# Optimization experiments

Hardware: AMD Instinct MI355X
Metric: run time of the kernel (lower is better)

## Reference

```python
import jax, jax.numpy as jnp
import numpy as np

N = 8192          # bbox_num
C = 2048          # in_channels
IC = C // 2       # inter_channels


def setup_inputs() -> dict:
    key = jax.random.key(0)
    ks = jax.random.split(key, 12)
    s_lin = 1.0 / np.sqrt(C)    # torch Linear init scale for fan_in=C
    s_w = 1.0 / np.sqrt(IC)     # for fan_in=IC
    return {
        "x": jax.random.normal(ks[0], (N, C), dtype=jnp.float32),
        "theta_w": jax.random.uniform(ks[1], (IC, C), jnp.float32, -s_lin, s_lin),
        "theta_b": jax.random.uniform(ks[2], (IC,), jnp.float32, -s_lin, s_lin),
        "phi_w": jax.random.uniform(ks[3], (IC, C), jnp.float32, -s_lin, s_lin),
        "phi_b": jax.random.uniform(ks[4], (IC,), jnp.float32, -s_lin, s_lin),
        "g_w": jax.random.uniform(ks[5], (IC, C), jnp.float32, -s_lin, s_lin),
        "g_b": jax.random.uniform(ks[6], (IC,), jnp.float32, -s_lin, s_lin),
        "W_w": jax.random.uniform(ks[7], (C, IC), jnp.float32, -s_w, s_w),
        "W_b": jax.random.uniform(ks[8], (C,), jnp.float32, -s_w, s_w),
        "mask_w": jax.random.uniform(ks[9], (N, C), jnp.float32, -s_lin, s_lin),
        "mask_b": jax.random.uniform(ks[10], (N,), jnp.float32, -s_lin, s_lin),
    }


def reference(x, theta_w, theta_b, phi_w, phi_b, g_w, g_b, W_w, W_b, mask_w, mask_b):
    # x: [N, C]. torch Linear: y = x @ W^T + b
    g_x = x @ g_w.T + g_b              # [N, IC]
    theta_x = x @ theta_w.T + theta_b  # [N, IC]
    phi_x = x @ phi_w.T + phi_b        # [N, IC]
    f = theta_x @ phi_x.T              # [N, N]
    # resize(): ad-hoc Linear(C -> N) then softmax over last dim
    mask = jax.nn.softmax(x @ mask_w.T + mask_b, axis=-1)  # [N, N]
    f = f * mask
    f_div_C = jax.nn.softmax(f, axis=-1)  # [N, N]
    y = f_div_C @ g_x                  # [N, IC]
    W_y = y @ W_w.T + W_b              # [N, C]
    z = W_y + x                        # residual
    return (z, f_div_C)
```

## Files before the change

### kernel.cpp

```cpp
#include <hip/hip_runtime.h>
#include <hip/hip_bf16.h>

typedef __bf16 bf16_t;
typedef __bf16 bf16x8 __attribute__((ext_vector_type(8)));
typedef float f32x4 __attribute__((ext_vector_type(4)));

#define GLOAD16(gp, lp) __builtin_amdgcn_global_load_lds(                      \
    (const __attribute__((address_space(1))) void*)(gp),                       \
    (__attribute__((address_space(3))) void*)(lp), 16, 0, 0)
#define BARRIER() asm volatile("s_barrier" ::: "memory")
#define VMC(n) asm volatile("s_waitcnt vmcnt(" #n ")" ::: "memory")
#define LGK0()                                                                 \
  do {                                                                         \
    asm volatile("s_waitcnt lgkmcnt(0)" ::: "memory");                         \
    __builtin_amdgcn_sched_barrier(0);                                         \
  } while (0)

__global__ __launch_bounds__(256) void cast_f32_bf16_k(
    const float* __restrict__ in, bf16_t* __restrict__ out, long n8) {
  long i = (long)blockIdx.x * blockDim.x + threadIdx.x;
  long stride = (long)gridDim.x * blockDim.x;
  for (; i < n8; i += stride) {
    long e = i * 8;
    float4 a = *(const float4*)(in + e);
    float4 b = *(const float4*)(in + e + 4);
    bf16x8 o;
    o[0] = (__bf16)a.x; o[1] = (__bf16)a.y; o[2] = (__bf16)a.z; o[3] = (__bf16)a.w;
    o[4] = (__bf16)b.x; o[5] = (__bf16)b.y; o[6] = (__bf16)b.z; o[7] = (__bf16)b.w;
    *(bf16x8*)(out + e) = o;
  }
}

template <int BIAS, bool MUL>
__global__ __launch_bounds__(512, 2) void gemm256(
    const bf16_t* __restrict__ A, const bf16_t* __restrict__ B,
    const float* __restrict__ bias, const bf16_t* __restrict__ mulm,
    bf16_t* __restrict__ out, int M, int N, int K) {
  __shared__ __align__(1024) char lds[131072];
  const int tid = threadIdx.x;
  const int gx = N >> 8;
  int bid = blockIdx.y * gx + blockIdx.x;
  const int nwg = gridDim.x * gridDim.y;
  const int cpx = nwg >> 3;
  bid = (bid & 7) * cpx + (bid >> 3);
  const long row0 = (long)(bid / gx) * 256;
  const long col0 = (long)(bid % gx) * 256;
  const long Kl = K;

  const int w = tid >> 6, lane = tid & 63;
  const int wm = w >> 2, wn = w & 3;
  const int fr = lane & 15, fq = lane >> 4;

  const int arow = (wm * 128 + fr) * 128;
  const int brow = 32768 + (wn * 64 + fr) * 128;
  const int sw0 = ((fq ^ (fr & 7)) << 4);
  const int sw1 = (((4 | fq) ^ (fr & 7)) << 4);

  const int r0 = tid >> 3;
  const int s0 = (tid & 7) ^ (r0 & 7);
  const bf16_t* Ap = A + (row0 + r0) * Kl + s0 * 8;
  const bf16_t* Bp = B + (col0 + r0) * Kl + s0 * 8;
  const int dstA = w * 1024;

#define STG_A(h, U)                                                            \
  {                                                                            \
    const bf16_t* s_ = Ap + (long)(h)*128 * Kl + (long)(U)*64;                 \
    char* d_ = lds + (((U)&1) * 65536) + (h)*16384 + dstA;                     \
    GLOAD16(s_, d_);                                                           \
    GLOAD16(s_ + 64 * Kl, d_ + 8192);                                          \
  }
#define STG_B(h, U)                                                            \
  {                                                                            \
    const bf16_t* s_ = Bp + (long)(h)*128 * Kl + (long)(U)*64;                 \
    char* d_ = lds + (((U)&1) * 65536) + 32768 + (h)*16384 + dstA;             \
    GLOAD16(s_, d_);                                                           \
    GLOAD16(s_ + 64 * Kl, d_ + 8192);                                          \
  }
#define RD_A(buf, s)                                                           \
  {                                                                            \
    _Pragma("unroll") for (int i = 0; i < 4; ++i) {                            \
      aS[i * 2] = *(const bf16x8*)((buf) + arow + ((s)*4 + i) * 2048 + sw0);   \
      aS[i * 2 + 1] =                                                          \
          *(const bf16x8*)((buf) + arow + ((s)*4 + i) * 2048 + sw1);           \
    }                                                                          \
  }
#define RD_B(dst, buf, s)                                                      \
  {                                                                            \
    _Pragma("unroll") for (int j = 0; j < 2; ++j) {                            \
      dst[j * 2] = *(const bf16x8*)((buf) + brow + ((s)*2 + j) * 2048 + sw0);  \
      dst[j * 2 + 1] =                                                         \
          *(const bf16x8*)((buf) + brow + ((s)*2 + j) * 2048 + sw1);           \
    }                                                                          \
  }
#define QUAD(BV, I0, J0)                                                       \
  {                                                                            \
    __builtin_amdgcn_s_setprio(1);                                             \
    _Pragma("unroll") for (int i = 0; i < 4; ++i)                              \
        _Pragma("unroll") for (int j = 0; j < 2; ++j)                          \
            _Pragma("unroll") for (int kk = 0; kk < 2; ++kk)                   \
                acc[I0 + i][J0 + j] = __builtin_amdgcn_mfma_f32_16x16x32_bf16( \
                    aS[i * 2 + kk], BV[j * 2 + kk], acc[I0 + i][J0 + j], 0, 0, \
                    0);                                                        \
    __builtin_amdgcn_s_setprio(0);                                             \
  }

  f32x4 acc[8][4] = {};
  bf16x8 aS[8], bA[4], bB[4];
  const int NT = K >> 6;

  STG_A(0, 0); STG_A(1, 0); STG_B(0, 0); STG_B(1, 0);

  for (int T = 0; T < NT; ++T) {
    char* buf = lds + (T & 1) * 65536;
    const bool ST = (T < NT - 1);
    VMC(0);
    BARRIER();
    if (ST) STG_A(0, T + 1);
    RD_A(buf, 0);
    RD_B(bA, buf, 0);
    LGK0();
    QUAD(bA, 0, 0);
    RD_B(bB, buf, 1);
    if (ST) STG_A(1, T + 1);
    LGK0();
    QUAD(bB, 0, 2);
    RD_A(buf, 1);
    if (ST) STG_B(0, T + 1);
    LGK0();
    QUAD(bB, 4, 2);
    if (ST) STG_B(1, T + 1);
    QUAD(bA, 4, 0);
  }
#undef STG_A
#undef STG_B
#undef RD_A
#undef RD_B
#undef QUAD

#pragma unroll
  for (int i = 0; i < 8; ++i)
#pragma unroll
    for (int j = 0; j < 4; ++j)
#pragma unroll
      for (int r = 0; r < 4; ++r) {
        long gi = row0 + wm * 128 + i * 16 + fq * 4 + r;
        long gj = col0 + wn * 64 + j * 16 + fr;
        float v = acc[i][j][r];
        if (BIAS == 1) v += bias[gj];
        long idx = gi * (long)N + gj;
        if (MUL) v *= (float)mulm[idx];
        out[idx] = (bf16_t)v;
      }
}

template <int BIAS, bool MUL, bool RES, bool OUTBF16, int GROUP>
__global__ __launch_bounds__(256) void gemm_nt(
    const bf16_t* __restrict__ A, const bf16_t* __restrict__ B,
    const float* __restrict__ bias, const bf16_t* __restrict__ mulm,
    const float* __restrict__ res, float* __restrict__ outf,
    bf16_t* __restrict__ outb, int M, int N, int K) {
  __shared__ bf16_t As[128 * 32];
  __shared__ bf16_t Bs[128 * 32];
  const int tid = threadIdx.x;
  const int gx = gridDim.x, gy = gridDim.y;
  const int n = blockIdx.y * gx + blockIdx.x;
  const int xcd = n & 7, q = n >> 3;
  int br, bc;
  if (GROUP == 0) { br = xcd + 8 * (q / gx); bc = q % gx; }
  else            { bc = xcd + 8 * (q / gy); br = q % gy; }
  const long row0 = (long)br * 128;
  const long col0 = (long)bc * 128;
  const int wid = tid >> 6, lane = tid & 63;
  const int wr = (wid >> 1) * 64;
  const int wc = (wid & 1) * 64;
  const int fr = lane & 15, fq = lane >> 4;
  const int sx = (fr >> 1) & 3;
  const int srow = tid >> 2;
  const int scol = ((tid & 3) ^ ((srow >> 1) & 3)) * 8;

  f32x4 acc[4][4] = {};

  const bf16_t* Ag = A + (row0 + srow) * (long)K + scol;
  const bf16_t* Bg = B + (col0 + srow) * (long)K + scol;
  const long k64 = 64L * K;
  bf16_t* ldsA = As + wid * 512;
  bf16_t* ldsB = Bs + wid * 512;

  for (int k0 = 0; k0 < K; k0 += 32) {
    GLOAD16(Ag + k0, ldsA);
    GLOAD16(Ag + k0 + k64, ldsA + 2048);
    GLOAD16(Bg + k0, ldsB);
    GLOAD16(Bg + k0 + k64, ldsB + 2048);
    __syncthreads();
    bf16x8 av[4], bv[4];
#pragma unroll
    for (int i = 0; i < 4; i++)
      av[i] = *(const bf16x8*)(As + (wr + i * 16 + fr) * 32 + ((fq ^ sx) << 3));
#pragma unroll
    for (int j = 0; j < 4; j++)
      bv[j] = *(const bf16x8*)(Bs + (wc + j * 16 + fr) * 32 + ((fq ^ sx) << 3));
#pragma unroll
    for (int i = 0; i < 4; i++)
#pragma unroll
      for (int j = 0; j < 4; j++)
        acc[i][j] = __builtin_amdgcn_mfma_f32_16x16x32_bf16(av[i], bv[j],
                                                            acc[i][j], 0, 0, 0);
    __syncthreads();
  }

#pragma unroll
  for (int i = 0; i < 4; i++) {
#pragma unroll
    for (int j = 0; j < 4; j++) {
#pragma unroll
      for (int r = 0; r < 4; r++) {
        long gi = row0 + wr + i * 16 + fq * 4 + r;
        long gj = col0 + wc + j * 16 + fr;
        float v = acc[i][j][r];
        if (BIAS == 1) v += bias[gj];
        if (BIAS == 2) v += bias[gi];
        long idx = gi * (long)N + gj;
        if (MUL) v *= (float)mulm[idx];
        if (RES) v += res[idx];
        if (OUTBF16) outb[idx] = (bf16_t)v;
        else outf[idx] = v;
      }
    }
  }
}

__global__ __launch_bounds__(256) void softmax_bf16_inplace(
    bf16_t* __restrict__ buf) {
  const long row = blockIdx.x;
  bf16_t* p = buf + row * 8192;
  const int t = threadIdx.x;
  float v[32];
#pragma unroll
  for (int i = 0; i < 4; i++) {
    bf16x8 raw = *(const bf16x8*)(p + t * 32 + i * 8);
#pragma unroll
    for (int j = 0; j < 8; j++) v[i * 8 + j] = (float)raw[j];
  }
  float m = -1e30f;
#pragma unroll
  for (int i = 0; i < 32; i++) m = fmaxf(m, v[i]);
  for (int off = 32; off; off >>= 1) m = fmaxf(m, __shfl_xor(m, off, 64));
  __shared__ float redm[4], reds[4];
  if ((t & 63) == 0) redm[t >> 6] = m;
  __syncthreads();
  m = fmaxf(fmaxf(redm[0], redm[1]), fmaxf(redm[2], redm[3]));
  float s = 0.f;
#pragma unroll
  for (int i = 0; i < 32; i++) {
    v[i] = __expf(v[i] - m);
    s += v[i];
  }
  for (int off = 32; off; off >>= 1) s += __shfl_xor(s, off, 64);
  if ((t & 63) == 0) reds[t >> 6] = s;
  __syncthreads();
  s = reds[0] + reds[1] + reds[2] + reds[3];
  float inv = 1.0f / s;
#pragma unroll
  for (int i = 0; i < 4; i++) {
    bf16x8 o;
#pragma unroll
    for (int j = 0; j < 8; j++) o[j] = (bf16_t)(v[i * 8 + j] * inv);
    *(bf16x8*)(p + t * 32 + i * 8) = o;
  }
}

__global__ __launch_bounds__(256) void softmax_f_k(bf16_t* __restrict__ fm,
                                                   float* __restrict__ outf) {
  const long row = blockIdx.x;
  bf16_t* p = fm + row * 8192;
  float* q = outf + row * 8192;
  const int t = threadIdx.x;
  float v[32];
#pragma unroll
  for (int i = 0; i < 4; i++) {
    bf16x8 raw = *(const bf16x8*)(p + t * 32 + i * 8);
#pragma unroll
    for (int j = 0; j < 8; j++) v[i * 8 + j] = (float)raw[j];
  }
  float m = -1e30f;
#pragma unroll
  for (int i = 0; i < 32; i++) m = fmaxf(m, v[i]);
  for (int off = 32; off; off >>= 1) m = fmaxf(m, __shfl_xor(m, off, 64));
  __shared__ float redm[4], reds[4];
  if ((t & 63) == 0) redm[t >> 6] = m;
  __syncthreads();
  m = fmaxf(fmaxf(redm[0], redm[1]), fmaxf(redm[2], redm[3]));
  float s = 0.f;
#pragma unroll
  for (int i = 0; i < 32; i++) {
    v[i] = __expf(v[i] - m);
    s += v[i];
  }
  for (int off = 32; off; off >>= 1) s += __shfl_xor(s, off, 64);
  if ((t & 63) == 0) reds[t >> 6] = s;
  __syncthreads();
  s = reds[0] + reds[1] + reds[2] + reds[3];
  float inv = 1.0f / s;
#pragma unroll
  for (int i = 0; i < 8; i++) {
    float4 o;
    o.x = v[i * 4 + 0] * inv;
    o.y = v[i * 4 + 1] * inv;
    o.z = v[i * 4 + 2] * inv;
    o.w = v[i * 4 + 3] * inv;
    *(float4*)(q + t * 32 + i * 4) = o;
  }
#pragma unroll
  for (int i = 0; i < 4; i++) {
    bf16x8 o;
#pragma unroll
    for (int j = 0; j < 8; j++) o[j] = (bf16_t)(v[i * 8 + j] * inv);
    *(bf16x8*)(p + t * 32 + i * 8) = o;
  }
}

extern "C" void kernel_launch(void* const* d_in, const int* in_sizes, int n_in,
                              void* d_out, int out_size, void* d_ws,
                              size_t ws_size, hipStream_t stream) {
  const int N = 8192, C = 2048, IC = 1024;
  const float* x = (const float*)d_in[0];
  const float* theta_w = (const float*)d_in[1];
  const float* theta_b = (const float*)d_in[2];
  const float* phi_w = (const float*)d_in[3];
  const float* phi_b = (const float*)d_in[4];
  const float* g_w = (const float*)d_in[5];
  const float* g_b = (const float*)d_in[6];
  const float* W_w = (const float*)d_in[7];
  const float* W_b = (const float*)d_in[8];
  const float* mask_w = (const float*)d_in[9];
  const float* mask_b = (const float*)d_in[10];

  float* z_out = (float*)d_out;
  float* f_out = z_out + (long)N * C;

  bf16_t* ML = (bf16_t*)f_out;
  bf16_t* th16 = (bf16_t*)z_out;
  bf16_t* ph16 = th16 + (long)N * IC;
  bf16_t* gT16 = ph16 + (long)N * IC;

  char* w = (char*)d_ws;
  bf16_t* xb = (bf16_t*)w;      w += (long)N * C * 2;
  bf16_t* mwb = (bf16_t*)w;     w += (long)N * C * 2;
  bf16_t* thwb = (bf16_t*)w;    w += (long)IC * C * 2;
  bf16_t* phwb = (bf16_t*)w;    w += (long)IC * C * 2;
  bf16_t* gwb = (bf16_t*)w;     w += (long)IC * C * 2;
  bf16_t* Wwb = (bf16_t*)w;     w += (long)C * IC * 2;
  bf16_t* fm = (bf16_t*)w;      w += (long)N * N * 2;
  bf16_t* y16 = (bf16_t*)w;     w += (long)N * IC * 2;

  cast_f32_bf16_k<<<8192, 256, 0, stream>>>(x, xb, (long)N * C / 8);
  cast_f32_bf16_k<<<8192, 256, 0, stream>>>(mask_w, mwb, (long)N * C / 8);
  cast_f32_bf16_k<<<1024, 256, 0, stream>>>(theta_w, thwb, (long)IC * C / 8);
  cast_f32_bf16_k<<<1024, 256, 0, stream>>>(phi_w, phwb, (long)IC * C / 8);
  cast_f32_bf16_k<<<1024, 256, 0, stream>>>(g_w, gwb, (long)IC * C / 8);
  cast_f32_bf16_k<<<1024, 256, 0, stream>>>(W_w, Wwb, (long)C * IC / 8);

  gemm_nt<1, false, false, true, 0><<<dim3(IC / 128, N / 128), 256, 0, stream>>>(
      xb, thwb, theta_b, nullptr, nullptr, nullptr, th16, N, IC, C);
  gemm_nt<1, false, false, true, 0><<<dim3(IC / 128, N / 128), 256, 0, stream>>>(
      xb, phwb, phi_b, nullptr, nullptr, nullptr, ph16, N, IC, C);
  gemm_nt<2, false, false, true, 1><<<dim3(N / 128, IC / 128), 256, 0, stream>>>(
      gwb, xb, g_b, nullptr, nullptr, nullptr, gT16, IC, N, C);
  gemm256<1, false><<<dim3(N / 256, N / 256), 512, 0, stream>>>(
      xb, mwb, mask_b, nullptr, ML, N, N, C);
  softmax_bf16_inplace<<<N, 256, 0, stream>>>(ML);
  gemm256<0, true><<<dim3(N / 256, N / 256), 512, 0, stream>>>(
      th16, ph16, nullptr, ML, fm, N, N, IC);
  softmax_f_k<<<N, 256, 0, stream>>>(fm, f_out);
  gemm_nt<0, false, false, true, 0><<<dim3(IC / 128, N / 128), 256, 0, stream>>>(
      fm, gT16, nullptr, nullptr, nullptr, nullptr, y16, N, IC, N);
  gemm_nt<1, false, true, false, 0><<<dim3(C / 128, N / 128), 256, 0, stream>>>(
      y16, Wwb, W_b, nullptr, x, z_out, nullptr, N, C, IC);
}
```

Baseline: 1.100 ms.

## Pipeline 256-tile GEMM loads deeper and fold mask softmax normalization into epilogue

```diff
diff --git a/kernel.cpp b/kernel.cpp
--- a/kernel.cpp
+++ b/kernel.cpp
@@ -31,10 +31,11 @@
   }
 }
 
-template <int BIAS, bool MUL>
-__global__ __launch_bounds__(512, 2) void gemm256(
+template <int BIAS, bool EMASK>
+__global__ __launch_bounds__(512, 2) void gemm256p(
     const bf16_t* __restrict__ A, const bf16_t* __restrict__ B,
-    const float* __restrict__ bias, const bf16_t* __restrict__ mulm,
+    const float* __restrict__ bias, const bf16_t* __restrict__ ml,
+    const float* __restrict__ mrow, const float* __restrict__ invrow,
     bf16_t* __restrict__ out, int M, int N, int K) {
   __shared__ __align__(1024) char lds[131072];
   const int tid = threadIdx.x;
@@ -51,45 +52,45 @@
   const int wm = w >> 2, wn = w & 3;
   const int fr = lane & 15, fq = lane >> 4;
 
-  const int arow = (wm * 128 + fr) * 128;
-  const int brow = 32768 + (wn * 64 + fr) * 128;
-  const int sw0 = ((fq ^ (fr & 7)) << 4);
-  const int sw1 = (((4 | fq) ^ (fr & 7)) << 4);
-
-  const int r0 = tid >> 3;
-  const int s0 = (tid & 7) ^ (r0 & 7);
-  const bf16_t* Ap = A + (row0 + r0) * Kl + s0 * 8;
-  const bf16_t* Bp = B + (col0 + r0) * Kl + s0 * 8;
-  const int dstA = w * 1024;
+  const int rowA0 = (wm * 128 + fr) * 128;
+  const int rowB0 = 32768 + (wn * 64 + fr) * 128;
+  const int sl0 = ((fq ^ (fr & 7)) << 4);
+  const int sl1 = (((4 | fq) ^ (fr & 7)) << 4);
+
+  const int srow = 8 * w + (lane >> 3);
+  const int schk = (lane & 7) ^ (lane >> 3);
+  const bf16_t* Asrc = A + (row0 + srow) * Kl + schk * 8;
+  const bf16_t* Bsrc = B + (col0 + srow) * Kl + schk * 8;
+  const int dstb = w * 1024;
 
 #define STG_A(h, U)                                                            \
   {                                                                            \
-    const bf16_t* s_ = Ap + (long)(h)*128 * Kl + (long)(U)*64;                 \
-    char* d_ = lds + (((U)&1) * 65536) + (h)*16384 + dstA;                     \
+    const bf16_t* s_ = Asrc + (long)(h)*128 * Kl + (long)(U)*64;               \
+    char* d_ = lds + (((U)&1) * 65536) + (h)*16384 + dstb;                     \
     GLOAD16(s_, d_);                                                           \
     GLOAD16(s_ + 64 * Kl, d_ + 8192);                                          \
   }
 #define STG_B(h, U)                                                            \
   {                                                                            \
-    const bf16_t* s_ = Bp + (long)(h)*128 * Kl + (long)(U)*64;                 \
-    char* d_ = lds + (((U)&1) * 65536) + 32768 + (h)*16384 + dstA;             \
+    const bf16_t* s_ = Bsrc + (long)(h)*128 * Kl + (long)(U)*64;               \
+    char* d_ = lds + (((U)&1) * 65536) + 32768 + (h)*16384 + dstb;             \
     GLOAD16(s_, d_);                                                           \
     GLOAD16(s_ + 64 * Kl, d_ + 8192);                                          \
   }
-#define RD_A(buf, s)                                                           \
+#define RDA(lo)                                                                \
   {                                                                            \
     _Pragma("unroll") for (int i = 0; i < 4; ++i) {                            \
-      aS[i * 2] = *(const bf16x8*)((buf) + arow + ((s)*4 + i) * 2048 + sw0);   \
-      aS[i * 2 + 1] =                                                          \
-          *(const bf16x8*)((buf) + arow + ((s)*4 + i) * 2048 + sw1);           \
+      const char* rb = buf + rowA0 + ((lo) ? 0 : 8192) + i * 2048;             \
+      aS[i * 2] = *(const bf16x8*)(rb + sl0);                                  \
+      aS[i * 2 + 1] = *(const bf16x8*)(rb + sl1);                              \
     }                                                                          \
   }
-#define RD_B(dst, buf, s)                                                      \
+#define RDB(dst, hi)                                                           \
   {                                                                            \
     _Pragma("unroll") for (int j = 0; j < 2; ++j) {                            \
-      dst[j * 2] = *(const bf16x8*)((buf) + brow + ((s)*2 + j) * 2048 + sw0);  \
-      dst[j * 2 + 1] =                                                         \
-          *(const bf16x8*)((buf) + brow + ((s)*2 + j) * 2048 + sw1);           \
+      const char* rb = buf + rowB0 + ((hi) ? 4096 : 0) + j * 2048;             \
+      dst[j * 2] = *(const bf16x8*)(rb + sl0);                                 \
+      dst[j * 2 + 1] = *(const bf16x8*)(rb + sl1);                             \
     }                                                                          \
   }
 #define QUAD(BV, I0, J0)                                                       \
@@ -105,36 +106,47 @@
   }
 
   f32x4 acc[8][4] = {};
-  bf16x8 aS[8], bA[4], bB[4];
+  bf16x8 aS[8], bLo[4], bHi[4];
   const int NT = K >> 6;
 
-  STG_A(0, 0); STG_A(1, 0); STG_B(0, 0); STG_B(1, 0);
+  STG_A(0, 0); STG_A(1, 0); STG_B(0, 0); STG_B(1, 0); STG_A(0, 1);
+  VMC(2);
+  BARRIER();
 
   for (int T = 0; T < NT; ++T) {
     char* buf = lds + (T & 1) * 65536;
-    const bool ST = (T < NT - 1);
-    VMC(0);
-    BARRIER();
-    if (ST) STG_A(0, T + 1);
-    RD_A(buf, 0);
-    RD_B(bA, buf, 0);
+    RDA(true);
+    RDB(bLo, false);
+    if (T < NT - 1) STG_A(1, T + 1);
+    BARRIER();
     LGK0();
-    QUAD(bA, 0, 0);
-    RD_B(bB, buf, 1);
-    if (ST) STG_A(1, T + 1);
+    QUAD(bLo, 0, 0);
+    BARRIER();
+    RDB(bHi, true);
+    if (T < NT - 1) STG_B(0, T + 1);
+    BARRIER();
     LGK0();
-    QUAD(bB, 0, 2);
-    RD_A(buf, 1);
-    if (ST) STG_B(0, T + 1);
+    QUAD(bHi, 0, 2);
+    BARRIER();
+    RDA(false);
+    if (T < NT - 1) STG_B(1, T + 1);
+    BARRIER();
     LGK0();
-    QUAD(bB, 4, 2);
-    if (ST) STG_B(1, T + 1);
-    QUAD(bA, 4, 0);
+    QUAD(bHi, 4, 2);
+    BARRIER();
+    if (T < NT - 2) {
+      STG_A(0, T + 2);
+      VMC(2);
+    } else if (T == NT - 2) {
+      VMC(0);
+    }
+    QUAD(bLo, 4, 0);
+    BARRIER();
   }
 #undef STG_A
 #undef STG_B
-#undef RD_A
-#undef RD_B
+#undef RDA
+#undef RDB
 #undef QUAD
 
 #pragma unroll
@@ -148,7 +160,7 @@
         float v = acc[i][j][r];
         if (BIAS == 1) v += bias[gj];
         long idx = gi * (long)N + gj;
-        if (MUL) v *= (float)mulm[idx];
+        if (EMASK) v *= __expf((float)ml[idx] - mrow[gi]) * invrow[gi];
         out[idx] = (bf16_t)v;
       }
 }
@@ -229,10 +241,11 @@
   }
 }
 
-__global__ __launch_bounds__(256) void softmax_bf16_inplace(
-    bf16_t* __restrict__ buf) {
+__global__ __launch_bounds__(256) void softmax_stats(
+    const bf16_t* __restrict__ buf, float* __restrict__ mrow,
+    float* __restrict__ invrow) {
   const long row = blockIdx.x;
-  bf16_t* p = buf + row * 8192;
+  const bf16_t* p = buf + row * 8192;
   const int t = threadIdx.x;
   float v[32];
 #pragma unroll
@@ -251,21 +264,14 @@
   m = fmaxf(fmaxf(redm[0], redm[1]), fmaxf(redm[2], redm[3]));
   float s = 0.f;
 #pragma unroll
-  for (int i = 0; i < 32; i++) {
-    v[i] = __expf(v[i] - m);
-    s += v[i];
-  }
+  for (int i = 0; i < 32; i++) s += __expf(v[i] - m);
   for (int off = 32; off; off >>= 1) s += __shfl_xor(s, off, 64);
   if ((t & 63) == 0) reds[t >> 6] = s;
   __syncthreads();
-  s = reds[0] + reds[1] + reds[2] + reds[3];
-  float inv = 1.0f / s;
-#pragma unroll
-  for (int i = 0; i < 4; i++) {
-    bf16x8 o;
-#pragma unroll
-    for (int j = 0; j < 8; j++) o[j] = (bf16_t)(v[i * 8 + j] * inv);
-    *(bf16x8*)(p + t * 32 + i * 8) = o;
+  if (t == 0) {
+    s = reds[0] + reds[1] + reds[2] + reds[3];
+    mrow[row] = m;
+    invrow[row] = 1.0f / s;
   }
 }
 
@@ -352,6 +358,8 @@
   bf16_t* Wwb = (bf16_t*)w;     w += (long)C * IC * 2;
   bf16_t* fm = (bf16_t*)w;      w += (long)N * N * 2;
   bf16_t* y16 = (bf16_t*)w;     w += (long)N * IC * 2;
+  float* mrowb = (float*)w;     w += (long)N * 4;
+  float* invrowb = (float*)w;   w += (long)N * 4;
 
   cast_f32_bf16_k<<<8192, 256, 0, stream>>>(x, xb, (long)N * C / 8);
   cast_f32_bf16_k<<<8192, 256, 0, stream>>>(mask_w, mwb, (long)N * C / 8);
@@ -366,11 +374,11 @@
       xb, phwb, phi_b, nullptr, nullptr, nullptr, ph16, N, IC, C);
   gemm_nt<2, false, false, true, 1><<<dim3(N / 128, IC / 128), 256, 0, stream>>>(
       gwb, xb, g_b, nullptr, nullptr, nullptr, gT16, IC, N, C);
-  gemm256<1, false><<<dim3(N / 256, N / 256), 512, 0, stream>>>(
-      xb, mwb, mask_b, nullptr, ML, N, N, C);
-  softmax_bf16_inplace<<<N, 256, 0, stream>>>(ML);
-  gemm256<0, true><<<dim3(N / 256, N / 256), 512, 0, stream>>>(
-      th16, ph16, nullptr, ML, fm, N, N, IC);
+  gemm256p<1, false><<<dim3(N / 256, N / 256), 512, 0, stream>>>(
+      xb, mwb, mask_b, nullptr, nullptr, nullptr, ML, N, N, C);
+  softmax_stats<<<N, 256, 0, stream>>>(ML, mrowb, invrowb);
+  gemm256p<0, true><<<dim3(N / 256, N / 256), 512, 0, stream>>>(
+      th16, ph16, nullptr, ML, mrowb, invrowb, fm, N, N, IC);
   softmax_f_k<<<N, 256, 0, stream>>>(fm, f_out);
   gemm_nt<0, false, false, true, 0><<<dim3(IC / 128, N / 128), 256, 0, stream>>>(
       fm, gT16, nullptr, nullptr, nullptr, nullptr, y16, N, IC, N);
```

After: 1.079 ms. 2.0% less time.

## Fuse theta/phi GEMMs, defer mask softmax normalization into epilogue, use 256-tile GEMM

Applied to the files above, without the earlier changes.

```diff
diff --git a/kernel.cpp b/kernel.cpp
--- a/kernel.cpp
+++ b/kernel.cpp
@@ -31,11 +31,13 @@
   }
 }
 
-template <int BIAS, bool MUL>
+template <int BIAS, bool EMASK, bool RES, bool OUTBF16>
 __global__ __launch_bounds__(512, 2) void gemm256(
-    const bf16_t* __restrict__ A, const bf16_t* __restrict__ B,
-    const float* __restrict__ bias, const bf16_t* __restrict__ mulm,
-    bf16_t* __restrict__ out, int M, int N, int K) {
+    const bf16_t* __restrict__ A, long lda, const bf16_t* __restrict__ B,
+    long ldb, const float* __restrict__ bias, const bf16_t* __restrict__ ml,
+    const float* __restrict__ mrow, const float* __restrict__ invrow,
+    const float* __restrict__ res, float* __restrict__ outf,
+    bf16_t* __restrict__ outb, int M, int N, int K) {
   __shared__ __align__(1024) char lds[131072];
   const int tid = threadIdx.x;
   const int gx = N >> 8;
@@ -45,7 +47,6 @@
   bid = (bid & 7) * cpx + (bid >> 3);
   const long row0 = (long)(bid / gx) * 256;
   const long col0 = (long)(bid % gx) * 256;
-  const long Kl = K;
 
   const int w = tid >> 6, lane = tid & 63;
   const int wm = w >> 2, wn = w & 3;
@@ -58,23 +59,23 @@
 
   const int r0 = tid >> 3;
   const int s0 = (tid & 7) ^ (r0 & 7);
-  const bf16_t* Ap = A + (row0 + r0) * Kl + s0 * 8;
-  const bf16_t* Bp = B + (col0 + r0) * Kl + s0 * 8;
+  const bf16_t* Ap = A + (row0 + r0) * lda + s0 * 8;
+  const bf16_t* Bp = B + (col0 + r0) * ldb + s0 * 8;
   const int dstA = w * 1024;
 
 #define STG_A(h, U)                                                            \
   {                                                                            \
-    const bf16_t* s_ = Ap + (long)(h)*128 * Kl + (long)(U)*64;                 \
+    const bf16_t* s_ = Ap + (long)(h)*128 * lda + (long)(U)*64;                \
     char* d_ = lds + (((U)&1) * 65536) + (h)*16384 + dstA;                     \
     GLOAD16(s_, d_);                                                           \
-    GLOAD16(s_ + 64 * Kl, d_ + 8192);                                          \
+    GLOAD16(s_ + 64 * lda, d_ + 8192);                                         \
   }
 #define STG_B(h, U)                                                            \
   {                                                                            \
-    const bf16_t* s_ = Bp + (long)(h)*128 * Kl + (long)(U)*64;                 \
+    const bf16_t* s_ = Bp + (long)(h)*128 * ldb + (long)(U)*64;                \
     char* d_ = lds + (((U)&1) * 65536) + 32768 + (h)*16384 + dstA;             \
     GLOAD16(s_, d_);                                                           \
-    GLOAD16(s_ + 64 * Kl, d_ + 8192);                                          \
+    GLOAD16(s_ + 64 * ldb, d_ + 8192);                                         \
   }
 #define RD_A(buf, s)                                                           \
   {                                                                            \
@@ -148,8 +149,10 @@
         float v = acc[i][j][r];
         if (BIAS == 1) v += bias[gj];
         long idx = gi * (long)N + gj;
-        if (MUL) v *= (float)mulm[idx];
-        out[idx] = (bf16_t)v;
+        if (EMASK) v *= __expf((float)ml[idx] - mrow[gi]) * invrow[gi];
+        if (RES) v += res[idx];
+        if (OUTBF16) outb[idx] = (bf16_t)v;
+        else outf[idx] = v;
       }
 }
 
@@ -229,10 +232,11 @@
   }
 }
 
-__global__ __launch_bounds__(256) void softmax_bf16_inplace(
-    bf16_t* __restrict__ buf) {
+__global__ __launch_bounds__(256) void softmax_stats(
+    const bf16_t* __restrict__ buf, float* __restrict__ mrow,
+    float* __restrict__ invrow) {
   const long row = blockIdx.x;
-  bf16_t* p = buf + row * 8192;
+  const bf16_t* p = buf + row * 8192;
   const int t = threadIdx.x;
   float v[32];
 #pragma unroll
@@ -251,21 +255,14 @@
   m = fmaxf(fmaxf(redm[0], redm[1]), fmaxf(redm[2], redm[3]));
   float s = 0.f;
 #pragma unroll
-  for (int i = 0; i < 32; i++) {
-    v[i] = __expf(v[i] - m);
-    s += v[i];
-  }
+  for (int i = 0; i < 32; i++) s += __expf(v[i] - m);
   for (int off = 32; off; off >>= 1) s += __shfl_xor(s, off, 64);
   if ((t & 63) == 0) reds[t >> 6] = s;
   __syncthreads();
-  s = reds[0] + reds[1] + reds[2] + reds[3];
-  float inv = 1.0f / s;
-#pragma unroll
-  for (int i = 0; i < 4; i++) {
-    bf16x8 o;
-#pragma unroll
-    for (int j = 0; j < 8; j++) o[j] = (bf16_t)(v[i * 8 + j] * inv);
-    *(bf16x8*)(p + t * 32 + i * 8) = o;
+  if (t == 0) {
+    s = reds[0] + reds[1] + reds[2] + reds[3];
+    mrow[row] = m;
+    invrow[row] = 1.0f / s;
   }
 }
 
@@ -339,9 +336,8 @@
   float* f_out = z_out + (long)N * C;
 
   bf16_t* ML = (bf16_t*)f_out;
-  bf16_t* th16 = (bf16_t*)z_out;
-  bf16_t* ph16 = th16 + (long)N * IC;
-  bf16_t* gT16 = ph16 + (long)N * IC;
+  bf16_t* thph16 = (bf16_t*)z_out;
+  bf16_t* gT16 = thph16 + (long)N * 2048;
 
   char* w = (char*)d_ws;
   bf16_t* xb = (bf16_t*)w;      w += (long)N * C * 2;
@@ -352,6 +348,9 @@
   bf16_t* Wwb = (bf16_t*)w;     w += (long)C * IC * 2;
   bf16_t* fm = (bf16_t*)w;      w += (long)N * N * 2;
   bf16_t* y16 = (bf16_t*)w;     w += (long)N * IC * 2;
+  float* mrowb = (float*)w;     w += (long)N * 4;
+  float* invrowb = (float*)w;   w += (long)N * 4;
+  float* thph_b = (float*)w;    w += (long)2 * IC * 4;
 
   cast_f32_bf16_k<<<8192, 256, 0, stream>>>(x, xb, (long)N * C / 8);
   cast_f32_bf16_k<<<8192, 256, 0, stream>>>(mask_w, mwb, (long)N * C / 8);
@@ -359,21 +358,25 @@
   cast_f32_bf16_k<<<1024, 256, 0, stream>>>(phi_w, phwb, (long)IC * C / 8);
   cast_f32_bf16_k<<<1024, 256, 0, stream>>>(g_w, gwb, (long)IC * C / 8);
   cast_f32_bf16_k<<<1024, 256, 0, stream>>>(W_w, Wwb, (long)C * IC / 8);
-
-  gemm_nt<1, false, false, true, 0><<<dim3(IC / 128, N / 128), 256, 0, stream>>>(
-      xb, thwb, theta_b, nullptr, nullptr, nullptr, th16, N, IC, C);
-  gemm_nt<1, false, false, true, 0><<<dim3(IC / 128, N / 128), 256, 0, stream>>>(
-      xb, phwb, phi_b, nullptr, nullptr, nullptr, ph16, N, IC, C);
+  hipMemcpyAsync(thph_b, theta_b, IC * 4, hipMemcpyDeviceToDevice, stream);
+  hipMemcpyAsync(thph_b + IC, phi_b, IC * 4, hipMemcpyDeviceToDevice, stream);
+
+  gemm256<1, false, false, true><<<dim3(2048 / 256, N / 256), 512, 0, stream>>>(
+      xb, C, thwb, C, thph_b, nullptr, nullptr, nullptr, nullptr, nullptr,
+      thph16, N, 2048, C);
   gemm_nt<2, false, false, true, 1><<<dim3(N / 128, IC / 128), 256, 0, stream>>>(
       gwb, xb, g_b, nullptr, nullptr, nullptr, gT16, IC, N, C);
-  gemm256<1, false><<<dim3(N / 256, N / 256), 512, 0, stream>>>(
-      xb, mwb, mask_b, nullptr, ML, N, N, C);
-  softmax_bf16_inplace<<<N, 256, 0, stream>>>(ML);
-  gemm256<0, true><<<dim3(N / 256, N / 256), 512, 0, stream>>>(
-      th16, ph16, nullptr, ML, fm, N, N, IC);
+  gemm256<1, false, false, true><<<dim3(N / 256, N / 256), 512, 0, stream>>>(
+      xb, C, mwb, C, mask_b, nullptr, nullptr, nullptr, nullptr, nullptr,
+      ML, N, N, C);
+  softmax_stats<<<N, 256, 0, stream>>>(ML, mrowb, invrowb);
+  gemm256<0, true, false, true><<<dim3(N / 256, N / 256), 512, 0, stream>>>(
+      thph16, 2048, thph16 + 1024, 2048, nullptr, ML, mrowb, invrowb,
+      nullptr, nullptr, fm, N, N, IC);
   softmax_f_k<<<N, 256, 0, stream>>>(fm, f_out);
   gemm_nt<0, false, false, true, 0><<<dim3(IC / 128, N / 128), 256, 0, stream>>>(
       fm, gT16, nullptr, nullptr, nullptr, nullptr, y16, N, IC, N);
-  gemm_nt<1, false, true, false, 0><<<dim3(C / 128, N / 128), 256, 0, stream>>>(
-      y16, Wwb, W_b, nullptr, x, z_out, nullptr, N, C, IC);
-}
+  gemm256<1, false, true, false><<<dim3(C / 256, N / 256), 512, 0, stream>>>(
+      y16, IC, Wwb, IC, W_b, nullptr, nullptr, nullptr, x, z_out, nullptr,
+      N, C, IC);
+}
```

Measured after the change: 1.010 ms. 1.09x faster.
